# Optimization experiments

Measured on AMD Instinct MI355X. Metric: run time of the kernel, lower is better.

Reference implementation:

```python
import jax, jax.numpy as jnp
import numpy as np

GROUPS = 32
EPS = 1e-5

def setup_inputs() -> dict:
    key = jax.random.key(0)
    ks = jax.random.split(key, 10)
    B, H, W, C = 2, 64, 64, 512
    s = 1.0 / np.sqrt(C)
    return {
        "x": jax.random.normal(ks[0], (B, H, W, C), dtype=jnp.float32),
        "gamma": jnp.ones((C,), jnp.float32),
        "beta": jnp.zeros((C,), jnp.float32),
        "wq": jax.random.normal(ks[1], (C, C), jnp.float32) * s,
        "bq": jnp.zeros((C,), jnp.float32),
        "wk": jax.random.normal(ks[2], (C, C), jnp.float32) * s,
        "bk": jnp.zeros((C,), jnp.float32),
        "wv": jax.random.normal(ks[3], (C, C), jnp.float32) * s,
        "bv": jnp.zeros((C,), jnp.float32),
        "wp": jax.random.normal(ks[4], (C, C), jnp.float32) * s,
        "bp": jnp.zeros((C,), jnp.float32),
    }

def _group_norm(x, gamma, beta):
    B, H, W, C = x.shape
    xg = x.reshape(B, H, W, GROUPS, C // GROUPS)
    mean = jnp.mean(xg, axis=(1, 2, 4), keepdims=True)
    var = jnp.var(xg, axis=(1, 2, 4), keepdims=True)
    xg = (xg - mean) * jax.lax.rsqrt(var + EPS)
    return xg.reshape(B, H, W, C) * gamma + beta

def reference(x, gamma, beta, wq, bq, wk, bk, wv, bv, wp, bp):
    B, H, W, C = x.shape
    h_ = _group_norm(x, gamma, beta)
    # 1x1 convs are per-pixel linear maps
    q = jnp.einsum("bhwc,cd->bhwd", h_, wq) + bq
    k = jnp.einsum("bhwc,cd->bhwd", h_, wk) + bk
    v = jnp.einsum("bhwc,cd->bhwd", h_, wv) + bv
    q = q.reshape(B, H * W, C)
    k = k.reshape(B, H * W, C)
    v = v.reshape(B, H * W, C)
    scale = C ** (-0.5)
    attn = jax.nn.softmax(jnp.einsum("bqc,bkc->bqk", q, k) * scale, axis=-1)
    out = jnp.einsum("bqk,bkc->bqc", attn, v).reshape(B, H, W, C)
    proj = jnp.einsum("bhwc,cd->bhwd", out, wp) + bp
    return x + proj
```

## Files before the change

kernel.cpp:

```cpp
#include <hip/hip_runtime.h>
#include <hip/hip_bf16.h>
#include <cstdint>
#include <cstddef>

typedef __bf16 bf16;
typedef bf16 bf16x8 __attribute__((ext_vector_type(8)));
typedef bf16 bf16x4 __attribute__((ext_vector_type(4)));
typedef float floatx4 __attribute__((ext_vector_type(4)));
typedef int intx8 __attribute__((ext_vector_type(8)));
typedef int intx4 __attribute__((ext_vector_type(4)));

#define DEVI __device__ __forceinline__

#define C_  512
#define HW_ 4096
#define B_  2
#define M_  8192
#define TK  64


DEVI floatx4 mfma16(bf16x8 a, bf16x8 b, floatx4 c) {
  return __builtin_amdgcn_mfma_f32_16x16x32_bf16(a, b, c, 0, 0, 0);
}

DEVI floatx4 mfma_fp8(intx8 a, intx8 b, floatx4 c) {
  return __builtin_amdgcn_mfma_scale_f32_16x16x128_f8f6f4(a, b, c, 0, 0,
                                                          0, 127, 0, 127);
}

DEVI void gload16(const void* g, void* lds) {
  using gp = const __attribute__((address_space(1))) unsigned int*;
  using lp = __attribute__((address_space(3))) unsigned int*;
  __builtin_amdgcn_global_load_lds(
      reinterpret_cast<gp>(reinterpret_cast<uintptr_t>(g)),
      reinterpret_cast<lp>((unsigned int)(uintptr_t)lds), 16, 0, 0);
}

DEVI uint32_t f32_to_fp8(float x) {
  return (uint32_t)__builtin_amdgcn_cvt_pk_fp8_f32(x, x, 0, false) & 0xffu;
}
DEVI int pack4_fp8(float a, float b, float c, float d) {
  int pk = __builtin_amdgcn_cvt_pk_fp8_f32(a, b, 0, false);
  return __builtin_amdgcn_cvt_pk_fp8_f32(c, d, pk, true);
}

__global__ __launch_bounds__(256) void gn_part(const float* __restrict__ x,
                                               float* __restrict__ pp,
                                               float* __restrict__ l) {
  int blk = blockIdx.x;
  int t = threadIdx.x;
  if (t < 16) l[blk * 16 + t] = 0.f;
  int batch = blk >> 8;
  int pix0 = (blk & 255) * 16;
  int c4 = (t & 127) << 2;
  int ph = t >> 7;
  const float* px = x + (size_t)batch * HW_ * C_ + (size_t)(pix0 + ph) * C_ + c4;
  float s1 = 0.f, s2 = 0.f;
#pragma unroll
  for (int i = 0; i < 8; i++) {
    float4 v = *reinterpret_cast<const float4*>(px + (size_t)i * 2 * C_);
    s1 += v.x + v.y + v.z + v.w;
    s2 += v.x * v.x + v.y * v.y + v.z * v.z + v.w * v.w;
  }
  __shared__ float l1[256], l2[256];
  l1[t] = s1; l2[t] = s2;
  __syncthreads();
  if (t < 32) {
    float a = 0.f, b2 = 0.f;
#pragma unroll
    for (int j = 0; j < 4; j++) {
      a  += l1[t * 4 + j] + l1[t * 4 + j + 128];
      b2 += l2[t * 4 + j] + l2[t * 4 + j + 128];
    }
    pp[blk * 32 + t] = a;
    pp[512 * 32 + blk * 32 + t] = b2;
  }
}

__global__ __launch_bounds__(256) void finish_wtrans(
    const float* __restrict__ pp, float* __restrict__ stats,
    const float* __restrict__ wq, const float* __restrict__ wk,
    const float* __restrict__ wv, const float* __restrict__ wp,
    uint8_t* __restrict__ w8, bf16* __restrict__ wtp) {
  int t = threadIdx.x;
  if (blockIdx.x < 64) {
    int bg = blockIdx.x;
    int b = bg >> 5, g = bg & 31;
    float s1 = pp[(b * 256 + t) * 32 + g];
    float s2 = pp[512 * 32 + (b * 256 + t) * 32 + g];
    for (int off = 32; off; off >>= 1) {
      s1 += __shfl_down(s1, off);
      s2 += __shfl_down(s2, off);
    }
    __shared__ float r1[4], r2[4];
    int wid = t >> 6;
    if ((t & 63) == 0) { r1[wid] = s1; r2[wid] = s2; }
    __syncthreads();
    if (t == 0) {
      s1 = r1[0] + r1[1] + r1[2] + r1[3];
      s2 = r2[0] + r2[1] + r2[2] + r2[3];
      float inv = 1.0f / (HW_ * 16);
      float mean = s1 * inv;
      float var  = s2 * inv - mean * mean;
      stats[bg]      = mean;
      stats[64 + bg] = rsqrtf(var + 1e-5f);
    }
    return;
  }
  int id = blockIdx.x - 64;
  int z = id >> 8;
  int k0 = ((id >> 4) & 15) * 32, n0 = (id & 15) * 32;
  const float* w = (z == 0) ? wq : (z == 1) ? wk : (z == 2) ? wv : wp;
  __shared__ float tt[32][33];
  int r = t >> 5, cc = t & 31;
  for (int i = 0; i < 4; i++) {
    int rr = r + i * 8;
    tt[rr][cc] = w[(size_t)(k0 + rr) * C_ + n0 + cc];
  }
  __syncthreads();
  if (z < 3) {
    uint8_t* dst = w8 + (size_t)z * C_ * C_;
    for (int i = 0; i < 4; i++) {
      int rr = r + i * 8;
      dst[(size_t)(n0 + rr) * C_ + k0 + cc] = (uint8_t)f32_to_fp8(tt[cc][rr]);
    }
  } else {
    for (int i = 0; i < 4; i++) {
      int rr = r + i * 8;
      wtp[(size_t)(n0 + rr) * C_ + k0 + cc] = (bf16)tt[cc][rr];
    }
  }
}

__global__ __launch_bounds__(256) void gn_apply(const float* __restrict__ x,
                                                const float* __restrict__ gamma,
                                                const float* __restrict__ beta,
                                                const float* __restrict__ stats,
                                                uint8_t* __restrict__ h8) {
  int idx = blockIdx.x * 256 + threadIdx.x;
  int m  = idx >> 7;
  int c4 = (idx & 127) << 2;
  int b = m >> 12;
  int g = c4 >> 4;
  float mean = stats[(b << 5) + g];
  float rs   = stats[64 + (b << 5) + g];
  const float4 xv = *reinterpret_cast<const float4*>(x + (size_t)m * C_ + c4);
  const float4 gv = *reinterpret_cast<const float4*>(gamma + c4);
  const float4 bv = *reinterpret_cast<const float4*>(beta + c4);
  int pk = pack4_fp8((xv.x - mean) * rs * gv.x + bv.x,
                     (xv.y - mean) * rs * gv.y + bv.y,
                     (xv.z - mean) * rs * gv.z + bv.z,
                     (xv.w - mean) * rs * gv.w + bv.w);
  *reinterpret_cast<int*>(h8 + (size_t)m * C_ + c4) = pk;
}

template <int BM, int BN, int MT, int NT>
DEVI void gemm_main(const bf16* __restrict__ A, int lda,
                    const bf16* __restrict__ Bt, int ldb,
                    int K, floatx4 (&acc)[MT][NT]) {
  constexpr int WCOLS = BN / (NT * 16);
  __shared__ __align__(16) bf16 As[BM * TK];
  __shared__ __align__(16) bf16 Bs[BN * TK];
  int tid = threadIdx.x;
  int w = tid >> 6, lane = tid & 63;
  int wrow = w / WCOLS, wcol = w % WCOLS;
  int col = lane & 15, quad = lane >> 4;
#pragma unroll
  for (int mt = 0; mt < MT; mt++)
#pragma unroll
    for (int nt = 0; nt < NT; nt++)
      acc[mt][nt] = floatx4{0.f, 0.f, 0.f, 0.f};
  for (int k0 = 0; k0 < K; k0 += TK) {
    __syncthreads();
#pragma unroll
    for (int i = 0; i < BM / 32; i++) {
      int id = tid + i * 256;
      int r = id >> 3, wd = id & 7;
      gload16(A + (size_t)r * lda + k0 + ((wd ^ (r & 7)) << 3), As + id * 8);
    }
#pragma unroll
    for (int i = 0; i < BN / 32; i++) {
      int id = tid + i * 256;
      int r = id >> 3, wd = id & 7;
      gload16(Bt + (size_t)r * ldb + k0 + ((wd ^ (r & 7)) << 3), Bs + id * 8);
    }
    __syncthreads();
#pragma unroll
    for (int kk = 0; kk < 2; kk++) {
      bf16x8 af[MT], bfr[NT];
#pragma unroll
      for (int mt = 0; mt < MT; mt++) {
        int rA = wrow * MT * 16 + mt * 16 + col;
        af[mt] = *reinterpret_cast<const bf16x8*>(
            As + rA * TK + (((kk * 4 + quad) ^ (rA & 7)) << 3));
      }
#pragma unroll
      for (int nt = 0; nt < NT; nt++) {
        int rB = wcol * NT * 16 + nt * 16 + col;
        bfr[nt] = *reinterpret_cast<const bf16x8*>(
            Bs + rB * TK + (((kk * 4 + quad) ^ (rB & 7)) << 3));
      }
#pragma unroll
      for (int mt = 0; mt < MT; mt++)
#pragma unroll
        for (int nt = 0; nt < NT; nt++)
          acc[mt][nt] = mfma16(af[mt], bfr[nt], acc[mt][nt]);
    }
  }
}

template <int BM, int BN, int MT, int NT>
DEVI void gemm_fp8(const uint8_t* __restrict__ A, int lda,
                   const uint8_t* __restrict__ Bt, int ldb,
                   int K, floatx4 (&acc)[MT][NT]) {
  constexpr int WCOLS = BN / (NT * 16);
  __shared__ __align__(16) uint8_t As[BM * 128];
  __shared__ __align__(16) uint8_t Bs[BN * 128];
  int tid = threadIdx.x;
  int w = tid >> 6, lane = tid & 63;
  int wrow = w / WCOLS, wcol = w % WCOLS;
  int col = lane & 15, quad = lane >> 4;
#pragma unroll
  for (int mt = 0; mt < MT; mt++)
#pragma unroll
    for (int nt = 0; nt < NT; nt++)
      acc[mt][nt] = floatx4{0.f, 0.f, 0.f, 0.f};
  for (int k0 = 0; k0 < K; k0 += 128) {
    __syncthreads();
#pragma unroll
    for (int i = 0; i < BM / 32; i++) {
      int id = tid + i * 256;
      int r = id >> 3, wd = id & 7;
      gload16(A + (size_t)r * lda + k0 + ((wd ^ (r & 7)) << 4), As + id * 16);
    }
#pragma unroll
    for (int i = 0; i < BN / 32; i++) {
      int id = tid + i * 256;
      int r = id >> 3, wd = id & 7;
      gload16(Bt + (size_t)r * ldb + k0 + ((wd ^ (r & 7)) << 4), Bs + id * 16);
    }
    __syncthreads();
    intx8 af[MT], bfr[NT];
#pragma unroll
    for (int mt = 0; mt < MT; mt++) {
      int rA = wrow * MT * 16 + mt * 16 + col;
      const uint8_t* rowp = As + (size_t)rA * 128;
      intx4 lo = *reinterpret_cast<const intx4*>(
          rowp + (((2 * quad) ^ (rA & 7)) << 4));
      intx4 hi = *reinterpret_cast<const intx4*>(
          rowp + (((2 * quad + 1) ^ (rA & 7)) << 4));
      af[mt] = __builtin_shufflevector(lo, hi, 0, 1, 2, 3, 4, 5, 6, 7);
    }
#pragma unroll
    for (int nt = 0; nt < NT; nt++) {
      int rB = wcol * NT * 16 + nt * 16 + col;
      const uint8_t* rowp = Bs + (size_t)rB * 128;
      intx4 lo = *reinterpret_cast<const intx4*>(
          rowp + (((2 * quad) ^ (rB & 7)) << 4));
      intx4 hi = *reinterpret_cast<const intx4*>(
          rowp + (((2 * quad + 1) ^ (rB & 7)) << 4));
      bfr[nt] = __builtin_shufflevector(lo, hi, 0, 1, 2, 3, 4, 5, 6, 7);
    }
#pragma unroll
    for (int mt = 0; mt < MT; mt++)
#pragma unroll
      for (int nt = 0; nt < NT; nt++)
        acc[mt][nt] = mfma_fp8(af[mt], bfr[nt], acc[mt][nt]);
  }
}

__global__ __launch_bounds__(256) void gemm_qkv(const uint8_t* __restrict__ h8,
                                                const uint8_t* __restrict__ w8,
                                                const float* __restrict__ bq,
                                                const float* __restrict__ bk,
                                                const float* __restrict__ bv,
                                                uint8_t* __restrict__ q8,
                                                uint8_t* __restrict__ k8,
                                                uint8_t* __restrict__ vt8) {
  int z = blockIdx.z;
  int m0 = blockIdx.x * 128, n0 = blockIdx.y * 64;
  floatx4 acc[2][4];
  gemm_fp8<128, 64, 2, 4>(h8 + (size_t)m0 * C_, C_,
                          w8 + (size_t)z * C_ * C_ + (size_t)n0 * C_, C_, C_, acc);
  int tid = threadIdx.x, w = tid >> 6, lane = tid & 63;
  int col = lane & 15, quad = lane >> 4;
  const float* bias = (z == 0) ? bq : (z == 1) ? bk : bv;
  if (z < 2) {
    uint8_t* out = (z == 0) ? q8 : k8;
#pragma unroll
    for (int mt = 0; mt < 2; mt++)
#pragma unroll
      for (int nt = 0; nt < 4; nt++) {
        int n = n0 + nt * 16 + col;
        float bb = bias[n];
#pragma unroll
        for (int r = 0; r < 4; r++) {
          int m = m0 + w * 32 + mt * 16 + quad * 4 + r;
          out[(size_t)m * C_ + n] = (uint8_t)f32_to_fp8(acc[mt][nt][r] + bb);
        }
      }
  } else {
#pragma unroll
    for (int mt = 0; mt < 2; mt++)
#pragma unroll
      for (int nt = 0; nt < 4; nt++) {
        int n = n0 + nt * 16 + col;
        float bb = bias[n];
        int mbase = m0 + w * 32 + mt * 16 + quad * 4;
        int b = mbase >> 12;
        int s = mbase & 4095;
        int pk = pack4_fp8(acc[mt][nt][0] + bb, acc[mt][nt][1] + bb,
                           acc[mt][nt][2] + bb, acc[mt][nt][3] + bb);
        *reinterpret_cast<int*>(vt8 + ((size_t)b * C_ + n) * HW_ + s) = pk;
      }
  }
}

__global__ __launch_bounds__(256) void gemm_qk(const uint8_t* __restrict__ q8,
                                               const uint8_t* __restrict__ k8,
                                               uint8_t* __restrict__ P8,
                                               float* __restrict__ l) {
  int b = blockIdx.z;
  int m0 = blockIdx.x * 128, n0 = blockIdx.y * 64;
  floatx4 acc[2][4];
  gemm_fp8<128, 64, 2, 4>(q8 + ((size_t)b * HW_ + m0) * C_, C_,
                          k8 + ((size_t)b * HW_ + n0) * C_, C_, C_, acc);
  int tid = threadIdx.x, w = tid >> 6, lane = tid & 63;
  int col = lane & 15, quad = lane >> 4;
  const float sl2e = 0.044194173824159216f * 1.4426950408889634f;
  uint8_t* Pb = P8 + (size_t)b * HW_ * HW_;
  float* lb = l + (size_t)b * HW_;
#pragma unroll
  for (int mt = 0; mt < 2; mt++) {
    float rs[4] = {0.f, 0.f, 0.f, 0.f};
#pragma unroll
    for (int nt = 0; nt < 4; nt++) {
      int n = n0 + nt * 16 + col;
      float p0 = exp2f(acc[mt][nt][0] * sl2e);
      float p1 = exp2f(acc[mt][nt][1] * sl2e);
      float p2 = exp2f(acc[mt][nt][2] * sl2e);
      float p3 = exp2f(acc[mt][nt][3] * sl2e);
      int pk = pack4_fp8(p0, p1, p2, p3);
      size_t base = (size_t)(m0 + w * 32 + mt * 16 + quad * 4) * HW_ + n;
      Pb[base]           = (uint8_t)pk;
      Pb[base + HW_]     = (uint8_t)((unsigned)pk >> 8);
      Pb[base + 2 * HW_] = (uint8_t)((unsigned)pk >> 16);
      Pb[base + 3 * HW_] = (uint8_t)((unsigned)pk >> 24);
      rs[0] += p0; rs[1] += p1; rs[2] += p2; rs[3] += p3;
    }
#pragma unroll
    for (int off = 1; off < 16; off <<= 1)
#pragma unroll
      for (int r = 0; r < 4; r++)
        rs[r] += __shfl_xor(rs[r], off);
    if (col == 0)
#pragma unroll
      for (int r = 0; r < 4; r++)
        atomicAdd(&lb[m0 + w * 32 + mt * 16 + quad * 4 + r], rs[r]);
  }
}

__global__ __launch_bounds__(256) void gemm_pv(const uint8_t* __restrict__ P8,
                                               const uint8_t* __restrict__ vt8,
                                               const float* __restrict__ l,
                                               bf16* __restrict__ o) {
  int b = blockIdx.z;
  int m0 = blockIdx.x * 128, n0 = blockIdx.y * 64;
  floatx4 acc[2][4];
  gemm_fp8<128, 64, 2, 4>(P8 + (size_t)b * HW_ * HW_ + (size_t)m0 * HW_, HW_,
                          vt8 + ((size_t)b * C_ + n0) * HW_, HW_, HW_, acc);
  int tid = threadIdx.x, w = tid >> 6, lane = tid & 63;
  int col = lane & 15, quad = lane >> 4;
  const float* lb = l + (size_t)b * HW_;
  bf16* ob = o + (size_t)b * HW_ * C_;
#pragma unroll
  for (int mt = 0; mt < 2; mt++)
#pragma unroll
    for (int r = 0; r < 4; r++) {
      int m = m0 + w * 32 + mt * 16 + quad * 4 + r;
      float inv = 1.0f / lb[m];
#pragma unroll
      for (int nt = 0; nt < 4; nt++) {
        int n = n0 + nt * 16 + col;
        ob[(size_t)m * C_ + n] = (bf16)(acc[mt][nt][r] * inv);
      }
    }
}

__global__ __launch_bounds__(256) void gemm_proj(const bf16* __restrict__ o,
                                                 const bf16* __restrict__ wtp,
                                                 const float* __restrict__ bp,
                                                 const float* __restrict__ x,
                                                 float* __restrict__ out) {
  int m0 = blockIdx.x * 128, n0 = blockIdx.y * 64;
  floatx4 acc[2][4];
  gemm_main<128, 64, 2, 4>(o + (size_t)m0 * C_, C_, wtp + (size_t)n0 * C_, C_, C_, acc);
  int tid = threadIdx.x, w = tid >> 6, lane = tid & 63;
  int col = lane & 15, quad = lane >> 4;
#pragma unroll
  for (int mt = 0; mt < 2; mt++)
#pragma unroll
    for (int nt = 0; nt < 4; nt++) {
      int n = n0 + nt * 16 + col;
      float bb = bp[n];
#pragma unroll
      for (int r = 0; r < 4; r++) {
        int m = m0 + w * 32 + mt * 16 + quad * 4 + r;
        out[(size_t)m * C_ + n] = x[(size_t)m * C_ + n] + acc[mt][nt][r] + bb;
      }
    }
}

extern "C" void kernel_launch(void* const* d_in, const int* in_sizes, int n_in,
                              void* d_out, int out_size, void* d_ws, size_t ws_size,
                              hipStream_t stream) {
  const float* x     = (const float*)d_in[0];
  const float* gamma = (const float*)d_in[1];
  const float* beta  = (const float*)d_in[2];
  const float* wq    = (const float*)d_in[3];
  const float* bq    = (const float*)d_in[4];
  const float* wk    = (const float*)d_in[5];
  const float* bk    = (const float*)d_in[6];
  const float* wv    = (const float*)d_in[7];
  const float* bv    = (const float*)d_in[8];
  const float* wp    = (const float*)d_in[9];
  const float* bp    = (const float*)d_in[10];
  float* out = (float*)d_out;

  char* w8s = (char*)d_ws;
  float* stats = (float*)(w8s);
  float* l     = (float*)(w8s + 65536u);
  float* pp    = (float*)(w8s + 393216u);
  uint8_t* w8  = (uint8_t*)(w8s + (1u << 20));
  bf16* wtp    = (bf16*)(w8s + (2u << 20));
  uint8_t* h8  = (uint8_t*)(w8s + (4u << 20));
  bf16* o      = (bf16*)(w8s + (8u << 20));
  uint8_t* q8  = (uint8_t*)(w8s + (16u << 20));
  uint8_t* k8  = (uint8_t*)(w8s + (20u << 20));
  uint8_t* vt8 = (uint8_t*)(w8s + (24u << 20));
  uint8_t* P8  = (uint8_t*)(w8s + (28u << 20));

  gn_part<<<512, 256, 0, stream>>>(x, pp, l);
  finish_wtrans<<<1088, 256, 0, stream>>>(pp, stats, wq, wk, wv, wp, w8, wtp);
  gn_apply<<<4096, 256, 0, stream>>>(x, gamma, beta, stats, h8);
  gemm_qkv<<<dim3(M_ / 128, C_ / 64, 3), 256, 0, stream>>>(h8, w8, bq, bk, bv, q8, k8, vt8);
  gemm_qk<<<dim3(HW_ / 128, HW_ / 64, B_), 256, 0, stream>>>(q8, k8, P8, l);
  gemm_pv<<<dim3(HW_ / 128, C_ / 64, B_), 256, 0, stream>>>(P8, vt8, l, o);
  gemm_proj<<<dim3(M_ / 128, C_ / 64, 1), 256, 0, stream>>>(o, wtp, bp, x, out);
}
```

Before: 183.9 us.

## Triple-buffer GEMM LDS loads with vmcnt waits and remap blocks for XCD locality

Both GEMM mainloops (bf16 and fp8) now use a three-stage LDS ring: loads for tile t+2 are issued before computing tile t, with explicit s_waitcnt vmcnt and s_barrier replacing the two __syncthreads per iteration. This is meant to hide global-to-LDS latency behind MFMA work. Block index mapping is also changed: the qkv and proj grids are transposed, and the qk and pv kernels swizzle block IDs so that blocks landing on the same XCD share A/B tiles in cache. In exchange, LDS use triples, which may lower occupancy, and the hand-written waitcnt logic is fragile if the compiler reorders or inserts its own memory ops.

```diff
diff --git a/kernel.cpp b/kernel.cpp
--- a/kernel.cpp
+++ b/kernel.cpp
@@ -34,6 +34,15 @@
   __builtin_amdgcn_global_load_lds(
       reinterpret_cast<gp>(reinterpret_cast<uintptr_t>(g)),
       reinterpret_cast<lp>((unsigned int)(uintptr_t)lds), 16, 0, 0);
+}
+
+template <int N> DEVI void wait_vmcnt() {
+  if constexpr (N == 0)       asm volatile("s_waitcnt vmcnt(0)" ::: "memory");
+  else if constexpr (N == 6)  asm volatile("s_waitcnt vmcnt(6)" ::: "memory");
+  else if constexpr (N == 8)  asm volatile("s_waitcnt vmcnt(8)" ::: "memory");
+  else if constexpr (N == 12) asm volatile("s_waitcnt vmcnt(12)" ::: "memory");
+  else if constexpr (N == 16) asm volatile("s_waitcnt vmcnt(16)" ::: "memory");
+  else static_assert(N == 0, "unsupported vmcnt literal");
 }
 
 DEVI uint32_t f32_to_fp8(float x) {
@@ -159,8 +168,10 @@
                     const bf16* __restrict__ Bt, int ldb,
                     int K, floatx4 (&acc)[MT][NT]) {
   constexpr int WCOLS = BN / (NT * 16);
-  __shared__ __align__(16) bf16 As[BM * TK];
-  __shared__ __align__(16) bf16 Bs[BN * TK];
+  constexpr int NLD = BM / 32 + BN / 32;
+  static_assert(NLD == 6 || NLD == 8, "vmcnt literals support 6/8");
+  __shared__ __align__(16) bf16 As[3][BM * TK];
+  __shared__ __align__(16) bf16 Bs[3][BN * TK];
   int tid = threadIdx.x;
   int w = tid >> 6, lane = tid & 63;
   int wrow = w / WCOLS, wcol = w % WCOLS;
@@ -170,21 +181,22 @@
 #pragma unroll
     for (int nt = 0; nt < NT; nt++)
       acc[mt][nt] = floatx4{0.f, 0.f, 0.f, 0.f};
-  for (int k0 = 0; k0 < K; k0 += TK) {
-    __syncthreads();
+
+  auto stage = [&](int k0, bf16* as, bf16* bs) {
 #pragma unroll
     for (int i = 0; i < BM / 32; i++) {
       int id = tid + i * 256;
       int r = id >> 3, wd = id & 7;
-      gload16(A + (size_t)r * lda + k0 + ((wd ^ (r & 7)) << 3), As + id * 8);
+      gload16(A + (size_t)r * lda + k0 + ((wd ^ (r & 7)) << 3), as + id * 8);
     }
 #pragma unroll
     for (int i = 0; i < BN / 32; i++) {
       int id = tid + i * 256;
       int r = id >> 3, wd = id & 7;
-      gload16(Bt + (size_t)r * ldb + k0 + ((wd ^ (r & 7)) << 3), Bs + id * 8);
-    }
-    __syncthreads();
+      gload16(Bt + (size_t)r * ldb + k0 + ((wd ^ (r & 7)) << 3), bs + id * 8);
+    }
+  };
+  auto compute = [&](const bf16* sa, const bf16* sb) {
 #pragma unroll
     for (int kk = 0; kk < 2; kk++) {
       bf16x8 af[MT], bfr[NT];
@@ -192,13 +204,13 @@
       for (int mt = 0; mt < MT; mt++) {
         int rA = wrow * MT * 16 + mt * 16 + col;
         af[mt] = *reinterpret_cast<const bf16x8*>(
-            As + rA * TK + (((kk * 4 + quad) ^ (rA & 7)) << 3));
+            sa + rA * TK + (((kk * 4 + quad) ^ (rA & 7)) << 3));
       }
 #pragma unroll
       for (int nt = 0; nt < NT; nt++) {
         int rB = wcol * NT * 16 + nt * 16 + col;
         bfr[nt] = *reinterpret_cast<const bf16x8*>(
-            Bs + rB * TK + (((kk * 4 + quad) ^ (rB & 7)) << 3));
+            sb + rB * TK + (((kk * 4 + quad) ^ (rB & 7)) << 3));
       }
 #pragma unroll
       for (int mt = 0; mt < MT; mt++)
@@ -206,6 +218,31 @@
         for (int nt = 0; nt < NT; nt++)
           acc[mt][nt] = mfma16(af[mt], bfr[nt], acc[mt][nt]);
     }
+  };
+
+  bf16 *a0 = &As[0][0], *a1 = &As[1][0], *a2 = &As[2][0];
+  bf16 *b0 = &Bs[0][0], *b1 = &Bs[1][0], *b2 = &Bs[2][0];
+  int nIter = K / TK;
+  stage(0, a0, b0);
+  stage(TK, a1, b1);
+  for (int t = 0; t < nIter; t++) {
+    if (t + 2 < nIter) {
+      stage((t + 2) * TK, a2, b2);
+      wait_vmcnt<2 * NLD>();
+    } else if (t + 1 < nIter) {
+      wait_vmcnt<NLD>();
+    } else {
+      wait_vmcnt<0>();
+    }
+    asm volatile("s_barrier" ::: "memory");
+    compute(a0, b0);
+    if (t + 1 < nIter) {
+      asm volatile("s_waitcnt lgkmcnt(0)" ::: "memory");
+      asm volatile("s_barrier" ::: "memory");
+    }
+    bf16* tp;
+    tp = a0; a0 = a1; a1 = a2; a2 = tp;
+    tp = b0; b0 = b1; b1 = b2; b2 = tp;
   }
 }
 
@@ -214,8 +251,10 @@
                    const uint8_t* __restrict__ Bt, int ldb,
                    int K, floatx4 (&acc)[MT][NT]) {
   constexpr int WCOLS = BN / (NT * 16);
-  __shared__ __align__(16) uint8_t As[BM * 128];
-  __shared__ __align__(16) uint8_t Bs[BN * 128];
+  constexpr int NLD = BM / 32 + BN / 32;
+  static_assert(NLD == 6 || NLD == 8, "vmcnt literals support 6/8");
+  __shared__ __align__(16) uint8_t As[3][BM * 128];
+  __shared__ __align__(16) uint8_t Bs[3][BN * 128];
   int tid = threadIdx.x;
   int w = tid >> 6, lane = tid & 63;
   int wrow = w / WCOLS, wcol = w % WCOLS;
@@ -225,26 +264,27 @@
 #pragma unroll
     for (int nt = 0; nt < NT; nt++)
       acc[mt][nt] = floatx4{0.f, 0.f, 0.f, 0.f};
-  for (int k0 = 0; k0 < K; k0 += 128) {
-    __syncthreads();
+
+  auto stage = [&](int k0, uint8_t* as, uint8_t* bs) {
 #pragma unroll
     for (int i = 0; i < BM / 32; i++) {
       int id = tid + i * 256;
       int r = id >> 3, wd = id & 7;
-      gload16(A + (size_t)r * lda + k0 + ((wd ^ (r & 7)) << 4), As + id * 16);
+      gload16(A + (size_t)r * lda + k0 + ((wd ^ (r & 7)) << 4), as + id * 16);
     }
 #pragma unroll
     for (int i = 0; i < BN / 32; i++) {
       int id = tid + i * 256;
       int r = id >> 3, wd = id & 7;
-      gload16(Bt + (size_t)r * ldb + k0 + ((wd ^ (r & 7)) << 4), Bs + id * 16);
-    }
-    __syncthreads();
+      gload16(Bt + (size_t)r * ldb + k0 + ((wd ^ (r & 7)) << 4), bs + id * 16);
+    }
+  };
+  auto compute = [&](const uint8_t* sa, const uint8_t* sb) {
     intx8 af[MT], bfr[NT];
 #pragma unroll
     for (int mt = 0; mt < MT; mt++) {
       int rA = wrow * MT * 16 + mt * 16 + col;
-      const uint8_t* rowp = As + (size_t)rA * 128;
+      const uint8_t* rowp = sa + (size_t)rA * 128;
       intx4 lo = *reinterpret_cast<const intx4*>(
           rowp + (((2 * quad) ^ (rA & 7)) << 4));
       intx4 hi = *reinterpret_cast<const intx4*>(
@@ -254,7 +294,7 @@
 #pragma unroll
     for (int nt = 0; nt < NT; nt++) {
       int rB = wcol * NT * 16 + nt * 16 + col;
-      const uint8_t* rowp = Bs + (size_t)rB * 128;
+      const uint8_t* rowp = sb + (size_t)rB * 128;
       intx4 lo = *reinterpret_cast<const intx4*>(
           rowp + (((2 * quad) ^ (rB & 7)) << 4));
       intx4 hi = *reinterpret_cast<const intx4*>(
@@ -266,6 +306,31 @@
 #pragma unroll
       for (int nt = 0; nt < NT; nt++)
         acc[mt][nt] = mfma_fp8(af[mt], bfr[nt], acc[mt][nt]);
+  };
+
+  uint8_t *a0 = &As[0][0], *a1 = &As[1][0], *a2 = &As[2][0];
+  uint8_t *b0 = &Bs[0][0], *b1 = &Bs[1][0], *b2 = &Bs[2][0];
+  int nIter = K >> 7;
+  stage(0, a0, b0);
+  stage(128, a1, b1);
+  for (int t = 0; t < nIter; t++) {
+    if (t + 2 < nIter) {
+      stage((t + 2) << 7, a2, b2);
+      wait_vmcnt<2 * NLD>();
+    } else if (t + 1 < nIter) {
+      wait_vmcnt<NLD>();
+    } else {
+      wait_vmcnt<0>();
+    }
+    asm volatile("s_barrier" ::: "memory");
+    compute(a0, b0);
+    if (t + 1 < nIter) {
+      asm volatile("s_waitcnt lgkmcnt(0)" ::: "memory");
+      asm volatile("s_barrier" ::: "memory");
+    }
+    uint8_t* tp;
+    tp = a0; a0 = a1; a1 = a2; a2 = tp;
+    tp = b0; b0 = b1; b1 = b2; b2 = tp;
   }
 }
 
@@ -278,7 +343,7 @@
                                                 uint8_t* __restrict__ k8,
                                                 uint8_t* __restrict__ vt8) {
   int z = blockIdx.z;
-  int m0 = blockIdx.x * 128, n0 = blockIdx.y * 64;
+  int m0 = blockIdx.y * 128, n0 = blockIdx.x * 64;
   floatx4 acc[2][4];
   gemm_fp8<128, 64, 2, 4>(h8 + (size_t)m0 * C_, C_,
                           w8 + (size_t)z * C_ * C_ + (size_t)n0 * C_, C_, C_, acc);
@@ -321,7 +386,9 @@
                                                uint8_t* __restrict__ P8,
                                                float* __restrict__ l) {
   int b = blockIdx.z;
-  int m0 = blockIdx.x * 128, n0 = blockIdx.y * 64;
+  int fid = blockIdx.y * 32 + blockIdx.x;
+  int nid = (fid & 7) * 256 + (fid >> 3);
+  int m0 = (nid & 31) * 128, n0 = (nid >> 5) * 64;
   floatx4 acc[2][4];
   gemm_fp8<128, 64, 2, 4>(q8 + ((size_t)b * HW_ + m0) * C_, C_,
                           k8 + ((size_t)b * HW_ + n0) * C_, C_, C_, acc);
@@ -365,7 +432,10 @@
                                                const float* __restrict__ l,
                                                bf16* __restrict__ o) {
   int b = blockIdx.z;
-  int m0 = blockIdx.x * 128, n0 = blockIdx.y * 64;
+  int fid = blockIdx.y * 32 + blockIdx.x;
+  int xcd = fid & 7, i = fid >> 3;
+  int m0 = (xcd * 4 + (i & 3)) * 128;
+  int n0 = (i >> 2) * 64;
   floatx4 acc[2][4];
   gemm_fp8<128, 64, 2, 4>(P8 + (size_t)b * HW_ * HW_ + (size_t)m0 * HW_, HW_,
                           vt8 + ((size_t)b * C_ + n0) * HW_, HW_, HW_, acc);
@@ -392,7 +462,7 @@
                                                  const float* __restrict__ bp,
                                                  const float* __restrict__ x,
                                                  float* __restrict__ out) {
-  int m0 = blockIdx.x * 128, n0 = blockIdx.y * 64;
+  int m0 = blockIdx.y * 128, n0 = blockIdx.x * 64;
   floatx4 acc[2][4];
   gemm_main<128, 64, 2, 4>(o + (size_t)m0 * C_, C_, wtp + (size_t)n0 * C_, C_, C_, acc);
   int tid = threadIdx.x, w = tid >> 6, lane = tid & 63;
@@ -443,8 +513,8 @@
   gn_part<<<512, 256, 0, stream>>>(x, pp, l);
   finish_wtrans<<<1088, 256, 0, stream>>>(pp, stats, wq, wk, wv, wp, w8, wtp);
   gn_apply<<<4096, 256, 0, stream>>>(x, gamma, beta, stats, h8);
-  gemm_qkv<<<dim3(M_ / 128, C_ / 64, 3), 256, 0, stream>>>(h8, w8, bq, bk, bv, q8, k8, vt8);
+  gemm_qkv<<<dim3(C_ / 64, M_ / 128, 3), 256, 0, stream>>>(h8, w8, bq, bk, bv, q8, k8, vt8);
   gemm_qk<<<dim3(HW_ / 128, HW_ / 64, B_), 256, 0, stream>>>(q8, k8, P8, l);
   gemm_pv<<<dim3(HW_ / 128, C_ / 64, B_), 256, 0, stream>>>(P8, vt8, l, o);
-  gemm_proj<<<dim3(M_ / 128, C_ / 64, 1), 256, 0, stream>>>(o, wtp, bp, x, out);
-}
+  gemm_proj<<<dim3(C_ / 64, M_ / 128, 1), 256, 0, stream>>>(o, wtp, bp, x, out);
+}
```

Result: slower. 193.2 us (+5.1%).
